# Kernel tuning notes

Hardware: AMD Instinct MI355X
Metric: run time of the kernel (lower is better)

## Reference

```python
import jax, jax.numpy as jnp
import numpy as np

B, Q, D, H, P, F = 16, 300, 256, 8, 4, 2048
HG = WG = 100          # feature-map height/width (hw = 10000, perfect square)
HW = HG * WG
DH = D // H
EPS = 1e-5


def _ln(x, g, b):
    m = x.mean(-1, keepdims=True)
    v = jnp.var(x, axis=-1, keepdims=True)
    return (x - m) * jax.lax.rsqrt(v + EPS) * g + b


def setup_inputs() -> dict:
    key = jax.random.key(0)
    ks = jax.random.split(key, 24)
    rn = lambda k, shape, s=0.02: jax.random.normal(k, shape, jnp.float32) * s
    return {
        "tgt": jax.random.normal(ks[0], (B, Q, D), jnp.float32),
        "memory": jax.random.normal(ks[1], (B, HW, D), jnp.float32),
        "in_proj_w": rn(ks[2], (D, 3 * D)), "in_proj_b": rn(ks[3], (3 * D,)),
        "out_proj_w": rn(ks[4], (D, D)), "out_proj_b": rn(ks[5], (D,)),
        "norm1_g": jnp.ones((D,), jnp.float32), "norm1_b": jnp.zeros((D,), jnp.float32),
        "ref_w": rn(ks[6], (D, 2)), "ref_b": rn(ks[7], (2,)),
        "off_w": rn(ks[8], (D, H * P * 2)), "off_b": rn(ks[9], (H * P * 2,)),
        "attw_w": rn(ks[10], (D, H * P)), "attw_b": rn(ks[11], (H * P,)),
        "vproj_w": rn(ks[12], (D, D)), "vproj_b": rn(ks[13], (D,)),
        "oproj_w": rn(ks[14], (D, D)), "oproj_b": rn(ks[15], (D,)),
        "norm2_g": jnp.ones((D,), jnp.float32), "norm2_b": jnp.zeros((D,), jnp.float32),
        "lin1_w": rn(ks[16], (D, F)), "lin1_b": rn(ks[17], (F,)),
        "lin2_w": rn(ks[18], (F, D)), "lin2_b": rn(ks[19], (D,)),
        "norm3_g": jnp.ones((D,), jnp.float32), "norm3_b": jnp.zeros((D,), jnp.float32),
    }


def reference(tgt, memory, in_proj_w, in_proj_b, out_proj_w, out_proj_b,
              norm1_g, norm1_b, ref_w, ref_b, off_w, off_b, attw_w, attw_b,
              vproj_w, vproj_b, oproj_w, oproj_b, norm2_g, norm2_b,
              lin1_w, lin1_b, lin2_w, lin2_b, norm3_g, norm3_b):
    # ---- self-attention (nn.MultiheadAttention, eval mode: dropout = identity)
    qkv = tgt @ in_proj_w + in_proj_b                      # [B,Q,3D]
    q, k, v = jnp.split(qkv, 3, axis=-1)
    q = q.reshape(B, Q, H, DH)
    k = k.reshape(B, Q, H, DH)
    v = v.reshape(B, Q, H, DH)
    scores = jnp.einsum('bqhd,bkhd->bhqk', q, k) / jnp.sqrt(jnp.float32(DH))
    attn = jax.nn.softmax(scores, axis=-1)
    sa = jnp.einsum('bhqk,bkhd->bqhd', attn, v).reshape(B, Q, D) @ out_proj_w + out_proj_b
    x = _ln(tgt + sa, norm1_g, norm1_b)

    # ---- reference points
    ref = jax.nn.sigmoid(x @ ref_w + ref_b)                # [B,Q,2] in (0,1)

    # ---- deformable cross-attention
    offs = (x @ off_w + off_b).reshape(B, Q, H, P, 2)
    wts = jax.nn.softmax((x @ attw_w + attw_b).reshape(B, Q, H, P), axis=-1)
    vals = (memory @ vproj_w + vproj_b).reshape(B, HW, H, DH)
    loc = jnp.clip(ref[:, :, None, None, :] + offs, 0.0, 1.0)
    sx = loc[..., 0] * (WG - 1)
    sy = loc[..., 1] * (HG - 1)
    x0 = jnp.floor(sx)
    y0 = jnp.floor(sy)
    x0i = jnp.clip(x0.astype(jnp.int32), 0, WG - 1)
    y0i = jnp.clip(y0.astype(jnp.int32), 0, HG - 1)
    x1i = jnp.clip(x0i + 1, 0, WG - 1)
    y1i = jnp.clip(y0i + 1, 0, HG - 1)
    wx1 = sx - x0
    wx0 = 1.0 - wx1
    wy1 = sy - y0
    wy0 = 1.0 - wy1
    bi = jnp.arange(B)[:, None, None, None]
    hi = jnp.arange(H)[None, None, :, None]

    def gather(yi, xi):                                    # [B,Q,H,P,DH]
        return vals[bi, yi * WG + xi, hi]

    samp = (gather(y0i, x0i) * (wx0 * wy0)[..., None]
            + gather(y1i, x0i) * (wx0 * wy1)[..., None]
            + gather(y0i, x1i) * (wx1 * wy0)[..., None]
            + gather(y1i, x1i) * (wx1 * wy1)[..., None])
    ca = (samp * wts[..., None]).sum(axis=3).reshape(B, Q, D) @ oproj_w + oproj_b
    x = _ln(x + ca, norm2_g, norm2_b)

    # ---- FFN
    ff = jax.nn.relu(x @ lin1_w + lin1_b) @ lin2_w + lin2_b
    return _ln(x + ff, norm3_g, norm3_b)
```

## Files before the change

### kernel.cpp

```cpp
#include <hip/hip_runtime.h>

#define NB   16
#define NQ   300
#define ND   256
#define NH   8
#define NP   4
#define NF   2048
#define NHW  10000
#define NWG  100
#define NROW 4800

typedef __attribute__((ext_vector_type(8))) short bf16x8;
typedef __attribute__((ext_vector_type(4))) float f32x4;

__device__ __forceinline__ unsigned short f2bf(float f) {
    unsigned u = __builtin_bit_cast(unsigned, f);
    u = (u + 0x7fffu + ((u >> 16) & 1u)) >> 16;
    return (unsigned short)u;
}
__device__ __forceinline__ float bf2f(unsigned short h) {
    unsigned u = ((unsigned)h) << 16;
    return __builtin_bit_cast(float, u);
}

__global__ __launch_bounds__(256) void prep_weights(
    const float* __restrict__ w_in,  const float* __restrict__ w_out,
    const float* __restrict__ w_vp,  const float* __restrict__ w_op,
    const float* __restrict__ w_l1,  const float* __restrict__ w_l2,
    const float* __restrict__ rw, const float* __restrict__ rb,
    const float* __restrict__ ow, const float* __restrict__ ob,
    const float* __restrict__ aw, const float* __restrict__ ab,
    unsigned short* __restrict__ o_in, unsigned short* __restrict__ o_out,
    unsigned short* __restrict__ o_vp, unsigned short* __restrict__ o_op,
    unsigned short* __restrict__ o_l1, unsigned short* __restrict__ o_l2,
    unsigned short* __restrict__ o_hd, float* __restrict__ o_hb)
{
    int id = blockIdx.x * 256 + threadIdx.x;
    if (id < 196608) {
        int n = id >> 8, k = id & 255;
        o_in[id] = f2bf(w_in[k * 768 + n]);  return;
    }
    id -= 196608;
    if (id < 65536) {
        int n = id >> 8, k = id & 255;
        o_out[id] = f2bf(w_out[k * 256 + n]); return;
    }
    id -= 65536;
    if (id < 65536) {
        int n = id >> 8, k = id & 255;
        o_vp[id] = f2bf(w_vp[k * 256 + n]);  return;
    }
    id -= 65536;
    if (id < 65536) {
        int n = id >> 8, k = id & 255;
        o_op[id] = f2bf(w_op[k * 256 + n]);  return;
    }
    id -= 65536;
    if (id < 524288) {
        int n = id >> 8, k = id & 255;
        o_l1[id] = f2bf(w_l1[k * 2048 + n]); return;
    }
    id -= 524288;
    if (id < 524288) {
        int n = id >> 11, k = id & 2047;
        o_l2[id] = f2bf(w_l2[k * 256 + n]);  return;
    }
    id -= 524288;
    if (id < 32768) {
        int n = id >> 8, k = id & 255;
        float v;
        if (n < 2)       v = rw[k * 2 + n];
        else if (n < 66) v = ow[k * 64 + (n - 2)];
        else if (n < 98) v = aw[k * 32 + (n - 66)];
        else             v = 0.0f;
        o_hd[id] = f2bf(v);                  return;
    }
    id -= 32768;
    if (id < 128) {
        float v;
        if (id < 2)       v = rb[id];
        else if (id < 66) v = ob[id - 2];
        else if (id < 98) v = ab[id - 66];
        else              v = 0.0f;
        o_hb[id] = v;
    }
}

template <int RELU, int OUTBF, int SPLITK>
__global__ __launch_bounds__(256, 3) void gemm_bt(
    const float* __restrict__ A, const unsigned short* __restrict__ Bt,
    const float* __restrict__ bias, void* __restrict__ Cout,
    int M, int N, int K)
{
    __shared__ unsigned short As[2][128][40];
    __shared__ unsigned short Bs[2][128][40];
    const int t    = threadIdx.x;
    const long m0  = (long)blockIdx.y * 128;
    const int  n0  = blockIdx.x * 128;
    const int  sr  = t >> 1;
    const int  sc  = (t & 1) << 4;
    const int  wave = t >> 6, lane = t & 63;
    const int  wm  = (wave >> 1) << 6;
    const int  wn  = (wave & 1) << 6;
    const int  l16 = lane & 15, quad = lane >> 4;

    f32x4 acc[4][4] = {};

    const bool aOk = (m0 + sr) < M;
    const float* aBase          = A  + (m0 + sr) * (long)K + sc;
    const unsigned short* bBase = Bt + (long)(n0 + sr) * K + sc;

    const int kChunk = K / SPLITK;
    const int kBeg   = (SPLITK > 1) ? blockIdx.z * kChunk : 0;
    const int nk     = kChunk / 32;

    float4 fa0, fa1, fa2, fa3;
    uint4  tb0, tb1;

    auto loadAB = [&](int kt) {
        const int k0 = kBeg + kt * 32;
        if (aOk) {
            const float4* ap = (const float4*)(aBase + k0);
            fa0 = ap[0]; fa1 = ap[1]; fa2 = ap[2]; fa3 = ap[3];
        } else {
            fa0 = make_float4(0, 0, 0, 0); fa1 = fa0; fa2 = fa0; fa3 = fa0;
        }
        const uint4* bp = (const uint4*)(bBase + k0);
        tb0 = bp[0]; tb1 = bp[1];
    };
    auto storeLDS = [&](int buf) {
        unsigned short ta[16];
        ta[0]  = f2bf(fa0.x); ta[1]  = f2bf(fa0.y); ta[2]  = f2bf(fa0.z); ta[3]  = f2bf(fa0.w);
        ta[4]  = f2bf(fa1.x); ta[5]  = f2bf(fa1.y); ta[6]  = f2bf(fa1.z); ta[7]  = f2bf(fa1.w);
        ta[8]  = f2bf(fa2.x); ta[9]  = f2bf(fa2.y); ta[10] = f2bf(fa2.z); ta[11] = f2bf(fa2.w);
        ta[12] = f2bf(fa3.x); ta[13] = f2bf(fa3.y); ta[14] = f2bf(fa3.z); ta[15] = f2bf(fa3.w);
        *(bf16x8*)&As[buf][sr][sc]     = *(bf16x8*)&ta[0];
        *(bf16x8*)&As[buf][sr][sc + 8] = *(bf16x8*)&ta[8];
        *(uint4*)&Bs[buf][sr][sc]      = tb0;
        *(uint4*)&Bs[buf][sr][sc + 8]  = tb1;
    };

    loadAB(0);
    storeLDS(0);
    __syncthreads();

    for (int kt = 0; kt < nk; kt++) {
        const int cur = kt & 1;
        if (kt + 1 < nk) loadAB(kt + 1);

        bf16x8 af[4], bfr[4];
        #pragma unroll
        for (int i = 0; i < 4; i++)
            af[i] = *(const bf16x8*)&As[cur][wm + i * 16 + l16][quad * 8];
        #pragma unroll
        for (int j = 0; j < 4; j++)
            bfr[j] = *(const bf16x8*)&Bs[cur][wn + j * 16 + l16][quad * 8];
        #pragma unroll
        for (int i = 0; i < 4; i++)
            #pragma unroll
            for (int j = 0; j < 4; j++)
                acc[i][j] = __builtin_amdgcn_mfma_f32_16x16x32_bf16(
                    bfr[j], af[i], acc[i][j], 0, 0, 0);

        if (kt + 1 < nk) {
            storeLDS(cur ^ 1);
            __syncthreads();
        }
    }

    float4 bj[4];
    #pragma unroll
    for (int j = 0; j < 4; j++)
        bj[j] = *(const float4*)&bias[n0 + wn + j * 16 + quad * 4];

    if (SPLITK > 1) {
        const float bscale = (blockIdx.z == 0) ? 1.0f : 0.0f;
        #pragma unroll
        for (int i = 0; i < 4; i++) {
            const long gr = m0 + wm + i * 16 + l16;
            if (gr < M) {
                #pragma unroll
                for (int j = 0; j < 4; j++) {
                    float* cp = (float*)Cout + gr * N + n0 + wn + j * 16 + quad * 4;
                    atomicAdd(cp + 0, acc[i][j][0] + bscale * bj[j].x);
                    atomicAdd(cp + 1, acc[i][j][1] + bscale * bj[j].y);
                    atomicAdd(cp + 2, acc[i][j][2] + bscale * bj[j].z);
                    atomicAdd(cp + 3, acc[i][j][3] + bscale * bj[j].w);
                }
            }
        }
        return;
    }

    #pragma unroll
    for (int i = 0; i < 4; i++) {
        const long gr = m0 + wm + i * 16 + l16;
        if (gr < M) {
            #pragma unroll
            for (int j = 0; j < 4; j++) {
                float4 v;
                v.x = acc[i][j][0] + bj[j].x;
                v.y = acc[i][j][1] + bj[j].y;
                v.z = acc[i][j][2] + bj[j].z;
                v.w = acc[i][j][3] + bj[j].w;
                if (RELU) {
                    v.x = fmaxf(v.x, 0.f); v.y = fmaxf(v.y, 0.f);
                    v.z = fmaxf(v.z, 0.f); v.w = fmaxf(v.w, 0.f);
                }
                const int gc = n0 + wn + j * 16 + quad * 4;
                if (OUTBF) {
                    unsigned short o[4] = {f2bf(v.x), f2bf(v.y), f2bf(v.z), f2bf(v.w)};
                    *(uint2*)((unsigned short*)Cout + gr * N + gc) = *(uint2*)o;
                } else {
                    *(float4*)((float*)Cout + gr * N + gc) = v;
                }
            }
        }
    }
}

__global__ __launch_bounds__(256) void attn_kernel(
    const float* __restrict__ qkv, float* __restrict__ sa)
{
    __shared__ union {
        struct {
            unsigned short Ks[304][40];
            unsigned short Qs[64][40];
        } s;
        unsigned short Ps[4][16][328];
    } u;
    __shared__ unsigned short Vt[32][328];

    const int bh = blockIdx.y;
    const int b  = bh >> 3, h = bh & 7;
    const int q0 = blockIdx.x * 64;
    const int t  = threadIdx.x;

    for (int idx = t; idx < 304 * 8; idx += 256) {
        const int r = idx >> 3, c4 = (idx & 7) << 2;
        if (r < NQ) {
            const float4 kv = *(const float4*)(qkv + ((long)(b * NQ + r)) * 768 + 256 + h * 32 + c4);
            u.s.Ks[r][c4 + 0] = f2bf(kv.x); u.s.Ks[r][c4 + 1] = f2bf(kv.y);
            u.s.Ks[r][c4 + 2] = f2bf(kv.z); u.s.Ks[r][c4 + 3] = f2bf(kv.w);
        } else {
            u.s.Ks[r][c4 + 0] = 0; u.s.Ks[r][c4 + 1] = 0;
            u.s.Ks[r][c4 + 2] = 0; u.s.Ks[r][c4 + 3] = 0;
        }
    }
    for (int idx = t; idx < NQ * 8; idx += 256) {
        const int key = idx >> 3, dq = (idx & 7) << 2;
        const float4 vv = *(const float4*)(qkv + ((long)(b * NQ + key)) * 768 + 512 + h * 32 + dq);
        Vt[dq + 0][key] = f2bf(vv.x); Vt[dq + 1][key] = f2bf(vv.y);
        Vt[dq + 2][key] = f2bf(vv.z); Vt[dq + 3][key] = f2bf(vv.w);
    }
    for (int idx = t; idx < 32 * 20; idx += 256)
        Vt[idx / 20][300 + idx % 20] = 0;
    for (int idx = t; idx < 64 * 8; idx += 256) {
        const int r = idx >> 3, c4 = (idx & 7) << 2;
        const int q = q0 + r;
        if (q < NQ) {
            const float4 qv = *(const float4*)(qkv + ((long)(b * NQ + q)) * 768 + h * 32 + c4);
            u.s.Qs[r][c4 + 0] = f2bf(qv.x); u.s.Qs[r][c4 + 1] = f2bf(qv.y);
            u.s.Qs[r][c4 + 2] = f2bf(qv.z); u.s.Qs[r][c4 + 3] = f2bf(qv.w);
        } else {
            u.s.Qs[r][c4 + 0] = 0; u.s.Qs[r][c4 + 1] = 0;
            u.s.Qs[r][c4 + 2] = 0; u.s.Qs[r][c4 + 3] = 0;
        }
    }
    __syncthreads();

    const int wave = t >> 6, lane = t & 63;
    const int l16 = lane & 15, quad = lane >> 4;
    const float scale = 0.1767766952966369f;

    const bf16x8 aq = *(const bf16x8*)&u.s.Qs[wave * 16 + l16][quad * 8];
    f32x4 sacc[19];
    #pragma unroll
    for (int kt = 0; kt < 19; kt++) {
        const bf16x8 bk = *(const bf16x8*)&u.s.Ks[kt * 16 + l16][quad * 8];
        sacc[kt] = __builtin_amdgcn_mfma_f32_16x16x32_bf16(
            aq, bk, (f32x4){0.f, 0.f, 0.f, 0.f}, 0, 0, 0);
    }

    float inv[4];
    #pragma unroll
    for (int r = 0; r < 4; r++) {
        float m = -1e30f;
        #pragma unroll
        for (int kt = 0; kt < 19; kt++) {
            float s = sacc[kt][r] * scale;
            if (kt == 18 && l16 >= 12) s = -1e30f;
            sacc[kt][r] = s;
            m = fmaxf(m, s);
        }
        m = fmaxf(m, __shfl_xor(m, 1)); m = fmaxf(m, __shfl_xor(m, 2));
        m = fmaxf(m, __shfl_xor(m, 4)); m = fmaxf(m, __shfl_xor(m, 8));
        float sum = 0.f;
        #pragma unroll
        for (int kt = 0; kt < 19; kt++) {
            float p = __expf(sacc[kt][r] - m);
            sacc[kt][r] = p;
            sum += p;
        }
        sum += __shfl_xor(sum, 1); sum += __shfl_xor(sum, 2);
        sum += __shfl_xor(sum, 4); sum += __shfl_xor(sum, 8);
        inv[r] = 1.0f / sum;
    }

    __syncthreads();

    #pragma unroll
    for (int kt = 0; kt < 19; kt++)
        #pragma unroll
        for (int r = 0; r < 4; r++)
            u.Ps[wave][quad * 4 + r][kt * 16 + l16] = f2bf(sacc[kt][r] * inv[r]);
    #pragma unroll
    for (int r = 0; r < 4; r++)
        u.Ps[wave][quad * 4 + r][304 + l16] = 0;

    f32x4 o0 = {0.f, 0.f, 0.f, 0.f}, o1 = {0.f, 0.f, 0.f, 0.f};
    #pragma unroll
    for (int kt = 0; kt < 10; kt++) {
        const bf16x8 ap  = *(const bf16x8*)&u.Ps[wave][l16][kt * 32 + quad * 8];
        const bf16x8 bv0 = *(const bf16x8*)&Vt[l16][kt * 32 + quad * 8];
        const bf16x8 bv1 = *(const bf16x8*)&Vt[16 + l16][kt * 32 + quad * 8];
        o0 = __builtin_amdgcn_mfma_f32_16x16x32_bf16(ap, bv0, o0, 0, 0, 0);
        o1 = __builtin_amdgcn_mfma_f32_16x16x32_bf16(ap, bv1, o1, 0, 0, 0);
    }

    #pragma unroll
    for (int r = 0; r < 4; r++) {
        const int q = q0 + wave * 16 + quad * 4 + r;
        if (q < NQ) {
            float* op = sa + ((long)(b * NQ + q)) * ND + h * 32;
            op[l16]      = o0[r];
            op[16 + l16] = o1[r];
        }
    }
}

__global__ __launch_bounds__(256) void residual_ln(
    const float* __restrict__ a, const float* __restrict__ r,
    const float* __restrict__ gam, const float* __restrict__ bet,
    float* __restrict__ out)
{
    const int row  = blockIdx.x * 4 + (threadIdx.x >> 6);
    const int lane = threadIdx.x & 63;
    const long base = (long)row * ND + lane * 4;
    float4 av = *(const float4*)(a + base);
    float4 rv = *(const float4*)(r + base);
    float x0 = av.x + rv.x, x1 = av.y + rv.y, x2 = av.z + rv.z, x3 = av.w + rv.w;
    float s  = x0 + x1 + x2 + x3;
    float s2 = x0 * x0 + x1 * x1 + x2 * x2 + x3 * x3;
    #pragma unroll
    for (int off = 32; off >= 1; off >>= 1) {
        s  += __shfl_xor(s, off);
        s2 += __shfl_xor(s2, off);
    }
    float mean = s * 0.00390625f;
    float var  = s2 * 0.00390625f - mean * mean;
    float rstd = rsqrtf(var + 1e-5f);
    float4 gv = *(const float4*)(gam + lane * 4);
    float4 bv = *(const float4*)(bet + lane * 4);
    float4 o;
    o.x = (x0 - mean) * rstd * gv.x + bv.x;
    o.y = (x1 - mean) * rstd * gv.y + bv.y;
    o.z = (x2 - mean) * rstd * gv.z + bv.z;
    o.w = (x3 - mean) * rstd * gv.w + bv.w;
    *(float4*)(out + base) = o;
}

__global__ __launch_bounds__(256) void meta_kernel(
    const float* __restrict__ res, float* __restrict__ meta)
{
    const int t   = threadIdx.x;
    const int row = blockIdx.x * 8 + (t >> 5);
    const int s   = t & 31;
    const int h   = s >> 2;
    const float* rp = res + (long)row * 128;
    const float rx = 1.f / (1.f + __expf(-rp[0]));
    const float ry = 1.f / (1.f + __expf(-rp[1]));
    const float offx = rp[2 + 2 * s], offy = rp[3 + 2 * s];
    const float a0 = rp[66 + h * 4 + 0], a1 = rp[66 + h * 4 + 1];
    const float a2 = rp[66 + h * 4 + 2], a3 = rp[66 + h * 4 + 3];
    const float mx = fmaxf(fmaxf(a0, a1), fmaxf(a2, a3));
    const float den = __expf(a0 - mx) + __expf(a1 - mx) +
                      __expf(a2 - mx) + __expf(a3 - mx);
    const float awt = __expf(rp[66 + s] - mx) / den;

    const float lx = fminf(fmaxf(rx + offx, 0.f), 1.f) * (NWG - 1);
    const float ly = fminf(fmaxf(ry + offy, 0.f), 1.f) * (NWG - 1);
    const float fx = floorf(lx), fy = floorf(ly);
    int x0 = (int)fx; x0 = min(max(x0, 0), NWG - 1);
    int y0 = (int)fy; y0 = min(max(y0, 0), NWG - 1);
    const int x1 = min(x0 + 1, NWG - 1);
    const int y1 = min(y0 + 1, NWG - 1);
    const float wx1 = lx - fx, wx0 = 1.f - wx1;
    const float wy1 = ly - fy, wy0 = 1.f - wy1;
    float4 m0, m1;
    m0.x = __int_as_float(y0 * NWG + x0);
    m0.y = __int_as_float(y0 * NWG + x1);
    m0.z = __int_as_float(y1 * NWG + x0);
    m0.w = __int_as_float(y1 * NWG + x1);
    m1.x = awt * wx0 * wy0;
    m1.y = awt * wx1 * wy0;
    m1.z = awt * wx0 * wy1;
    m1.w = awt * wx1 * wy1;
    float* mp = meta + (long)row * 256 + s * 8;
    *(float4*)mp       = m0;
    *(float4*)(mp + 4) = m1;
}

__global__ __launch_bounds__(256) void deform_gather(
    const float* __restrict__ meta, const unsigned short* __restrict__ vals,
    float* __restrict__ ca)
{
    const int row = blockIdx.x;
    const int b = row / NQ;
    __shared__ float ms[256];
    const int t = threadIdx.x;
    ms[t] = meta[(long)row * 256 + t];
    __syncthreads();
    const int h = t >> 5, d = t & 31;
    const unsigned short* vb = vals + (long)b * NHW * ND + h * 32 + d;
    float acc = 0.f;
    #pragma unroll
    for (int p = 0; p < NP; p++) {
        const float* mp = ms + h * 32 + p * 8;
        const int i00 = __float_as_int(mp[0]);
        const int i01 = __float_as_int(mp[1]);
        const int i10 = __float_as_int(mp[2]);
        const int i11 = __float_as_int(mp[3]);
        acc += mp[4] * bf2f(vb[(long)i00 * ND]);
        acc += mp[5] * bf2f(vb[(long)i01 * ND]);
        acc += mp[6] * bf2f(vb[(long)i10 * ND]);
        acc += mp[7] * bf2f(vb[(long)i11 * ND]);
    }
    ca[(long)row * ND + t] = acc;
}

extern "C" void kernel_launch(void* const* d_in, const int* in_sizes, int n_in,
                              void* d_out, int out_size, void* d_ws, size_t ws_size,
                              hipStream_t stream)
{
    (void)in_sizes; (void)n_in; (void)out_size; (void)ws_size;
    const float* tgt   = (const float*)d_in[0];
    const float* mem   = (const float*)d_in[1];
    const float* inpw  = (const float*)d_in[2];
    const float* inpb  = (const float*)d_in[3];
    const float* outw  = (const float*)d_in[4];
    const float* outb  = (const float*)d_in[5];
    const float* n1g   = (const float*)d_in[6];
    const float* n1b   = (const float*)d_in[7];
    const float* refw  = (const float*)d_in[8];
    const float* refb  = (const float*)d_in[9];
    const float* offw  = (const float*)d_in[10];
    const float* offb  = (const float*)d_in[11];
    const float* attww = (const float*)d_in[12];
    const float* attwb = (const float*)d_in[13];
    const float* vpw   = (const float*)d_in[14];
    const float* vpb   = (const float*)d_in[15];
    const float* opw   = (const float*)d_in[16];
    const float* opb   = (const float*)d_in[17];
    const float* n2g   = (const float*)d_in[18];
    const float* n2b   = (const float*)d_in[19];
    const float* l1w   = (const float*)d_in[20];
    const float* l1b   = (const float*)d_in[21];
    const float* l2w   = (const float*)d_in[22];
    const float* l2b   = (const float*)d_in[23];
    const float* n3g   = (const float*)d_in[24];
    const float* n3b   = (const float*)d_in[25];
    float* out = (float*)d_out;

    char* p = (char*)d_ws;
    auto alloc = [&](size_t bytes) {
        char* r = p; p += (bytes + 255) & ~(size_t)255; return (void*)r;
    };
    unsigned short* wtIn   = (unsigned short*)alloc(768 * 256 * 2);
    unsigned short* wtOut  = (unsigned short*)alloc(256 * 256 * 2);
    unsigned short* wtVp   = (unsigned short*)alloc(256 * 256 * 2);
    unsigned short* wtOp   = (unsigned short*)alloc(256 * 256 * 2);
    unsigned short* wtL1   = (unsigned short*)alloc(2048 * 256 * 2);
    unsigned short* wtL2   = (unsigned short*)alloc(256 * 2048 * 2);
    unsigned short* wtHead = (unsigned short*)alloc(128 * 256 * 2);
    float*          headb  = (float*)alloc(128 * 4);
    float* qkv  = (float*)alloc((size_t)NROW * 768 * 4);
    float* sa   = (float*)alloc((size_t)NROW * ND * 4);
    float* x1   = (float*)alloc((size_t)NROW * ND * 4);
    float* x2   = (float*)alloc((size_t)NROW * ND * 4);
    float* tmp  = (float*)alloc((size_t)NROW * ND * 4);
    float* ca   = (float*)alloc((size_t)NROW * ND * 4);
    float* meta = (float*)alloc((size_t)NROW * 256 * 4);
    void* uni = alloc((size_t)NB * NHW * ND * 2);
    unsigned short* vals = (unsigned short*)uni;
    float* h1 = (float*)uni;
    float* res = qkv;

    prep_weights<<<5761, 256, 0, stream>>>(
        inpw, outw, vpw, opw, l1w, l2w,
        refw, refb, offw, offb, attww, attwb,
        wtIn, wtOut, wtVp, wtOp, wtL1, wtL2, wtHead, headb);

    gemm_bt<0, 0, 1><<<dim3(6, 38), 256, 0, stream>>>(tgt, wtIn, inpb, qkv,
                                                      NROW, 768, 256);
    gemm_bt<0, 1, 1><<<dim3(2, 1250), 256, 0, stream>>>(mem, wtVp, vpb, vals,
                                                        NB * NHW, 256, 256);
    attn_kernel<<<dim3(5, 128), 256, 0, stream>>>(qkv, sa);
    gemm_bt<0, 0, 1><<<dim3(2, 38), 256, 0, stream>>>(sa, wtOut, outb, tmp,
                                                      NROW, 256, 256);
    residual_ln<<<1200, 256, 0, stream>>>(tgt, tmp, n1g, n1b, x1);
    gemm_bt<0, 0, 1><<<dim3(1, 38), 256, 0, stream>>>(x1, wtHead, headb, res,
                                                      NROW, 128, 256);
    meta_kernel<<<600, 256, 0, stream>>>(res, meta);
    deform_gather<<<4800, 256, 0, stream>>>(meta, vals, ca);
    gemm_bt<0, 0, 1><<<dim3(2, 38), 256, 0, stream>>>(ca, wtOp, opb, tmp,
                                                      NROW, 256, 256);
    residual_ln<<<1200, 256, 0, stream>>>(x1, tmp, n2g, n2b, x2);
    gemm_bt<1, 0, 1><<<dim3(16, 38), 256, 0, stream>>>(x2, wtL1, l1b, h1,
                                                       NROW, 2048, 256);
    hipMemsetAsync(tmp, 0, (size_t)NROW * ND * 4, stream);
    gemm_bt<0, 0, 4><<<dim3(2, 38, 4), 256, 0, stream>>>(h1, wtL2, l2b, tmp,
                                                         NROW, 256, 2048);
    residual_ln<<<1200, 256, 0, stream>>>(x2, tmp, n3g, n3b, out);
}
```

Baseline: 544.4 us.

## Use LDS-tiled weight transpose and 64-row GEMM tiles for small-M GEMMs

Replaces the per-element strided weight transpose/cast with a 64x64 shared-memory tiled transpose so reads and writes are coalesced, and splits the head-weight prep into its own kernel. Templates the GEMM on the M tile size and uses 64-row tiles with higher occupancy for the 4800-row GEMMs, roughly doubling the block count on a 256-CU part. The large value-projection GEMM keeps 128-row tiles. The load mapping also changes to spread loads across threads. Smaller tiles lower per-block reuse of B tiles.

```diff
diff --git a/kernel.cpp b/kernel.cpp
--- a/kernel.cpp
+++ b/kernel.cpp
@@ -23,49 +23,52 @@
     return __builtin_bit_cast(float, u);
 }
 
-__global__ __launch_bounds__(256) void prep_weights(
+__global__ __launch_bounds__(256) void transpose_cast(
     const float* __restrict__ w_in,  const float* __restrict__ w_out,
     const float* __restrict__ w_vp,  const float* __restrict__ w_op,
     const float* __restrict__ w_l1,  const float* __restrict__ w_l2,
+    unsigned short* __restrict__ o_in, unsigned short* __restrict__ o_out,
+    unsigned short* __restrict__ o_vp, unsigned short* __restrict__ o_op,
+    unsigned short* __restrict__ o_l1, unsigned short* __restrict__ o_l2)
+{
+    __shared__ float ts[64][65];
+    int b = blockIdx.x;
+    const float* src; unsigned short* dst; int K, N, ncx;
+    if      (b < 48)  { src = w_in;  dst = o_in;  K = 256;  N = 768;  ncx = 12; }
+    else if (b < 64)  { src = w_out; dst = o_out; K = 256;  N = 256;  ncx = 4;  b -= 48; }
+    else if (b < 80)  { src = w_vp;  dst = o_vp;  K = 256;  N = 256;  ncx = 4;  b -= 64; }
+    else if (b < 96)  { src = w_op;  dst = o_op;  K = 256;  N = 256;  ncx = 4;  b -= 80; }
+    else if (b < 224) { src = w_l1;  dst = o_l1;  K = 256;  N = 2048; ncx = 32; b -= 96; }
+    else              { src = w_l2;  dst = o_l2;  K = 2048; N = 256;  ncx = 4;  b -= 224; }
+    const int n0 = (b % ncx) * 64, k0 = (b / ncx) * 64;
+    const int t = threadIdx.x;
+    const int r = t >> 4, c = t & 15;
+    #pragma unroll
+    for (int j = 0; j < 4; j++) {
+        float4 v = *(const float4*)(src + (long)(k0 + j * 16 + r) * N + n0 + c * 4);
+        ts[j * 16 + r][c * 4 + 0] = v.x;
+        ts[j * 16 + r][c * 4 + 1] = v.y;
+        ts[j * 16 + r][c * 4 + 2] = v.z;
+        ts[j * 16 + r][c * 4 + 3] = v.w;
+    }
+    __syncthreads();
+    #pragma unroll
+    for (int j = 0; j < 4; j++) {
+        unsigned short o[4];
+        #pragma unroll
+        for (int i = 0; i < 4; i++)
+            o[i] = f2bf(ts[c * 4 + i][j * 16 + r]);
+        *(uint2*)(dst + (long)(n0 + j * 16 + r) * K + k0 + c * 4) = *(uint2*)o;
+    }
+}
+
+__global__ __launch_bounds__(256) void prep_head(
     const float* __restrict__ rw, const float* __restrict__ rb,
     const float* __restrict__ ow, const float* __restrict__ ob,
     const float* __restrict__ aw, const float* __restrict__ ab,
-    unsigned short* __restrict__ o_in, unsigned short* __restrict__ o_out,
-    unsigned short* __restrict__ o_vp, unsigned short* __restrict__ o_op,
-    unsigned short* __restrict__ o_l1, unsigned short* __restrict__ o_l2,
     unsigned short* __restrict__ o_hd, float* __restrict__ o_hb)
 {
     int id = blockIdx.x * 256 + threadIdx.x;
-    if (id < 196608) {
-        int n = id >> 8, k = id & 255;
-        o_in[id] = f2bf(w_in[k * 768 + n]);  return;
-    }
-    id -= 196608;
-    if (id < 65536) {
-        int n = id >> 8, k = id & 255;
-        o_out[id] = f2bf(w_out[k * 256 + n]); return;
-    }
-    id -= 65536;
-    if (id < 65536) {
-        int n = id >> 8, k = id & 255;
-        o_vp[id] = f2bf(w_vp[k * 256 + n]);  return;
-    }
-    id -= 65536;
-    if (id < 65536) {
-        int n = id >> 8, k = id & 255;
-        o_op[id] = f2bf(w_op[k * 256 + n]);  return;
-    }
-    id -= 65536;
-    if (id < 524288) {
-        int n = id >> 8, k = id & 255;
-        o_l1[id] = f2bf(w_l1[k * 2048 + n]); return;
-    }
-    id -= 524288;
-    if (id < 524288) {
-        int n = id >> 11, k = id & 2047;
-        o_l2[id] = f2bf(w_l2[k * 256 + n]);  return;
-    }
-    id -= 524288;
     if (id < 32768) {
         int n = id >> 8, k = id & 255;
         float v;
@@ -73,7 +76,8 @@
         else if (n < 66) v = ow[k * 64 + (n - 2)];
         else if (n < 98) v = aw[k * 32 + (n - 66)];
         else             v = 0.0f;
-        o_hd[id] = f2bf(v);                  return;
+        o_hd[id] = f2bf(v);
+        return;
     }
     id -= 32768;
     if (id < 128) {
@@ -86,58 +90,57 @@
     }
 }
 
-template <int RELU, int OUTBF, int SPLITK>
-__global__ __launch_bounds__(256, 3) void gemm_bt(
+template <int RELU, int OUTBF, int SPLITK, int TM>
+__global__ __launch_bounds__(256, (TM == 64) ? 4 : 3) void gemm_bt(
     const float* __restrict__ A, const unsigned short* __restrict__ Bt,
     const float* __restrict__ bias, void* __restrict__ Cout,
     int M, int N, int K)
 {
-    __shared__ unsigned short As[2][128][40];
+    constexpr int AI = TM / 32;
+    constexpr int NI = TM / 32;
+    __shared__ unsigned short As[2][TM][40];
     __shared__ unsigned short Bs[2][128][40];
     const int t    = threadIdx.x;
-    const long m0  = (long)blockIdx.y * 128;
+    const long m0  = (long)blockIdx.y * TM;
     const int  n0  = blockIdx.x * 128;
-    const int  sr  = t >> 1;
-    const int  sc  = (t & 1) << 4;
     const int  wave = t >> 6, lane = t & 63;
-    const int  wm  = (wave >> 1) << 6;
+    const int  wm  = (wave >> 1) * (TM / 2);
     const int  wn  = (wave & 1) << 6;
     const int  l16 = lane & 15, quad = lane >> 4;
-
-    f32x4 acc[4][4] = {};
-
-    const bool aOk = (m0 + sr) < M;
-    const float* aBase          = A  + (m0 + sr) * (long)K + sc;
-    const unsigned short* bBase = Bt + (long)(n0 + sr) * K + sc;
+    const int  arow = t >> 3, acol = (t & 7) << 2;
+    const int  brow = t >> 2, bcol = (t & 3) << 3;
+
+    f32x4 acc[NI][4] = {};
 
     const int kChunk = K / SPLITK;
     const int kBeg   = (SPLITK > 1) ? blockIdx.z * kChunk : 0;
     const int nk     = kChunk / 32;
 
-    float4 fa0, fa1, fa2, fa3;
-    uint4  tb0, tb1;
+    float4 fa[AI];
+    uint4  fb[2];
 
     auto loadAB = [&](int kt) {
         const int k0 = kBeg + kt * 32;
-        if (aOk) {
-            const float4* ap = (const float4*)(aBase + k0);
-            fa0 = ap[0]; fa1 = ap[1]; fa2 = ap[2]; fa3 = ap[3];
-        } else {
-            fa0 = make_float4(0, 0, 0, 0); fa1 = fa0; fa2 = fa0; fa3 = fa0;
-        }
-        const uint4* bp = (const uint4*)(bBase + k0);
-        tb0 = bp[0]; tb1 = bp[1];
+        #pragma unroll
+        for (int j = 0; j < AI; j++) {
+            const long r = m0 + j * 32 + arow;
+            fa[j] = (r < M) ? *(const float4*)(A + r * (long)K + k0 + acol)
+                            : make_float4(0.f, 0.f, 0.f, 0.f);
+        }
+        #pragma unroll
+        for (int j = 0; j < 2; j++)
+            fb[j] = *(const uint4*)(Bt + (long)(n0 + j * 64 + brow) * K + k0 + bcol);
     };
     auto storeLDS = [&](int buf) {
-        unsigned short ta[16];
-        ta[0]  = f2bf(fa0.x); ta[1]  = f2bf(fa0.y); ta[2]  = f2bf(fa0.z); ta[3]  = f2bf(fa0.w);
-        ta[4]  = f2bf(fa1.x); ta[5]  = f2bf(fa1.y); ta[6]  = f2bf(fa1.z); ta[7]  = f2bf(fa1.w);
-        ta[8]  = f2bf(fa2.x); ta[9]  = f2bf(fa2.y); ta[10] = f2bf(fa2.z); ta[11] = f2bf(fa2.w);
-        ta[12] = f2bf(fa3.x); ta[13] = f2bf(fa3.y); ta[14] = f2bf(fa3.z); ta[15] = f2bf(fa3.w);
-        *(bf16x8*)&As[buf][sr][sc]     = *(bf16x8*)&ta[0];
-        *(bf16x8*)&As[buf][sr][sc + 8] = *(bf16x8*)&ta[8];
-        *(uint4*)&Bs[buf][sr][sc]      = tb0;
-        *(uint4*)&Bs[buf][sr][sc + 8]  = tb1;
+        #pragma unroll
+        for (int j = 0; j < AI; j++) {
+            unsigned short ta[4] = {f2bf(fa[j].x), f2bf(fa[j].y),
+                                    f2bf(fa[j].z), f2bf(fa[j].w)};
+            *(uint2*)&As[buf][j * 32 + arow][acol] = *(uint2*)ta;
+        }
+        #pragma unroll
+        for (int j = 0; j < 2; j++)
+            *(uint4*)&Bs[buf][j * 64 + brow][bcol] = fb[j];
     };
 
     loadAB(0);
@@ -148,15 +151,15 @@
         const int cur = kt & 1;
         if (kt + 1 < nk) loadAB(kt + 1);
 
-        bf16x8 af[4], bfr[4];
-        #pragma unroll
-        for (int i = 0; i < 4; i++)
+        bf16x8 af[NI], bfr[4];
+        #pragma unroll
+        for (int i = 0; i < NI; i++)
             af[i] = *(const bf16x8*)&As[cur][wm + i * 16 + l16][quad * 8];
         #pragma unroll
         for (int j = 0; j < 4; j++)
             bfr[j] = *(const bf16x8*)&Bs[cur][wn + j * 16 + l16][quad * 8];
         #pragma unroll
-        for (int i = 0; i < 4; i++)
+        for (int i = 0; i < NI; i++)
             #pragma unroll
             for (int j = 0; j < 4; j++)
                 acc[i][j] = __builtin_amdgcn_mfma_f32_16x16x32_bf16(
@@ -176,7 +179,7 @@
     if (SPLITK > 1) {
         const float bscale = (blockIdx.z == 0) ? 1.0f : 0.0f;
         #pragma unroll
-        for (int i = 0; i < 4; i++) {
+        for (int i = 0; i < NI; i++) {
             const long gr = m0 + wm + i * 16 + l16;
             if (gr < M) {
                 #pragma unroll
@@ -193,7 +196,7 @@
     }
 
     #pragma unroll
-    for (int i = 0; i < 4; i++) {
+    for (int i = 0; i < NI; i++) {
         const long gr = m0 + wm + i * 16 + l16;
         if (gr < M) {
             #pragma unroll
@@ -496,30 +499,31 @@
     float* h1 = (float*)uni;
     float* res = qkv;
 
-    prep_weights<<<5761, 256, 0, stream>>>(
+    transpose_cast<<<352, 256, 0, stream>>>(
         inpw, outw, vpw, opw, l1w, l2w,
-        refw, refb, offw, offb, attww, attwb,
-        wtIn, wtOut, wtVp, wtOp, wtL1, wtL2, wtHead, headb);
-
-    gemm_bt<0, 0, 1><<<dim3(6, 38), 256, 0, stream>>>(tgt, wtIn, inpb, qkv,
-                                                      NROW, 768, 256);
-    gemm_bt<0, 1, 1><<<dim3(2, 1250), 256, 0, stream>>>(mem, wtVp, vpb, vals,
-                                                        NB * NHW, 256, 256);
+        wtIn, wtOut, wtVp, wtOp, wtL1, wtL2);
+    prep_head<<<129, 256, 0, stream>>>(refw, refb, offw, offb, attww, attwb,
+                                       wtHead, headb);
+
+    gemm_bt<0, 0, 1, 64><<<dim3(6, 75), 256, 0, stream>>>(tgt, wtIn, inpb, qkv,
+                                                          NROW, 768, 256);
+    gemm_bt<0, 1, 1, 128><<<dim3(2, 1250), 256, 0, stream>>>(mem, wtVp, vpb, vals,
+                                                             NB * NHW, 256, 256);
     attn_kernel<<<dim3(5, 128), 256, 0, stream>>>(qkv, sa);
-    gemm_bt<0, 0, 1><<<dim3(2, 38), 256, 0, stream>>>(sa, wtOut, outb, tmp,
-                                                      NROW, 256, 256);
+    gemm_bt<0, 0, 1, 64><<<dim3(2, 75), 256, 0, stream>>>(sa, wtOut, outb, tmp,
+                                                          NROW, 256, 256);
     residual_ln<<<1200, 256, 0, stream>>>(tgt, tmp, n1g, n1b, x1);
-    gemm_bt<0, 0, 1><<<dim3(1, 38), 256, 0, stream>>>(x1, wtHead, headb, res,
-                                                      NROW, 128, 256);
+    gemm_bt<0, 0, 1, 64><<<dim3(1, 75), 256, 0, stream>>>(x1, wtHead, headb, res,
+                                                          NROW, 128, 256);
     meta_kernel<<<600, 256, 0, stream>>>(res, meta);
     deform_gather<<<4800, 256, 0, stream>>>(meta, vals, ca);
-    gemm_bt<0, 0, 1><<<dim3(2, 38), 256, 0, stream>>>(ca, wtOp, opb, tmp,
-                                                      NROW, 256, 256);
+    gemm_bt<0, 0, 1, 64><<<dim3(2, 75), 256, 0, stream>>>(ca, wtOp, opb, tmp,
+                                                          NROW, 256, 256);
     residual_ln<<<1200, 256, 0, stream>>>(x1, tmp, n2g, n2b, x2);
-    gemm_bt<1, 0, 1><<<dim3(16, 38), 256, 0, stream>>>(x2, wtL1, l1b, h1,
-                                                       NROW, 2048, 256);
+    gemm_bt<1, 0, 1, 64><<<dim3(16, 75), 256, 0, stream>>>(x2, wtL1, l1b, h1,
+                                                           NROW, 2048, 256);
     hipMemsetAsync(tmp, 0, (size_t)NROW * ND * 4, stream);
-    gemm_bt<0, 0, 4><<<dim3(2, 38, 4), 256, 0, stream>>>(h1, wtL2, l2b, tmp,
-                                                         NROW, 256, 2048);
+    gemm_bt<0, 0, 4, 64><<<dim3(2, 75, 4), 256, 0, stream>>>(h1, wtL2, l2b, tmp,
+                                                             NROW, 256, 2048);
     residual_ln<<<1200, 256, 0, stream>>>(x2, tmp, n3g, n3b, out);
 }
```

Measured after the change: 577.1 us. 1.06x slower.
